# Kernel optimization log

Hardware: AMD Instinct MI355X
Metric: run time of the kernel (lower is better)

The kernel has to match this reference:

```python
import jax, jax.numpy as jnp
import numpy as np

H = 1024
N_IDX = 400000
NBINS = 256


def setup_inputs() -> dict:
    key = jax.random.key(0)
    ks = jax.random.split(key, 10)
    return {
        "input_data": jax.random.uniform(ks[0], (1, 3, H, H), jnp.float32),
        "target_data": jax.random.uniform(ks[1], (1, 3, H, H), jnp.float32) * 2.0 - 1.0,
        "ref": jax.random.uniform(ks[2], (1, 3, H, H), jnp.float32) * 2.0 - 1.0,
        "mask_src": (jax.random.uniform(ks[3], (1, 1, H, H)) > 0.3).astype(jnp.float32) * 255.0,
        "mask_tar": (jax.random.uniform(ks[4], (1, 1, H, H)) > 0.3).astype(jnp.float32) * 255.0,
        "target_data_eye": jax.random.uniform(ks[5], (1, 3, H, H), jnp.float32),
        "idx0": jax.random.randint(ks[6], (N_IDX,), 0, H),
        "idx1": jax.random.randint(ks[7], (N_IDX,), 0, H),
        "idx2": jax.random.randint(ks[8], (N_IDX,), 0, H),
        "idx3": jax.random.randint(ks[9], (N_IDX,), 0, H),
    }


def _cdf(vals):
    # vals: [3, N] float in [0, 256). torch.histc(bins=256, min=0, max=256) -> bin = floor(v)
    bins = jnp.clip(vals.astype(jnp.int32), 0, NBINS - 1)  # [3, N]
    hist = jnp.zeros((3, NBINS), jnp.float32).at[jnp.arange(3)[:, None], bins].add(1.0)
    cdf = jnp.cumsum(hist, axis=1)
    return cdf / cdf[:, -1:]  # normalized cumulative histogram, [3, 256]


def _trans_table(cdf_dst, cdf_ref):
    # cal_trans(ref=cdf_dst, adj=cdf_ref): table[i] = first j in [1,255]
    # with cdf_ref[j-1] <= cdf_dst[i] <= cdf_ref[j]; else table[i] = i; table[255] = 255
    r = cdf_dst[:, None]                  # [256, 1]
    lo = cdf_ref[None, :-1]               # [1, 255] -> adj[j-1], j = 1..255
    hi = cdf_ref[None, 1:]                # [1, 255] -> adj[j]
    cond = (r >= lo) & (r <= hi)          # [256, 255]
    has = cond.any(axis=1)
    j = jnp.argmax(cond, axis=1) + 1      # first matching j
    table = jnp.where(has, j, jnp.arange(NBINS))
    return table.at[NBINS - 1].set(NBINS - 1)


def _hist_match(dst_img, ref_img, i0, i1, i2, i3):
    # dst_img, ref_img: [3, H, W]; gather masked pixels per channel
    dst_align = dst_img[:, i0, i1]        # [3, N]
    ref_align = ref_img[:, i2, i3]        # [3, N]
    cdf_dst = _cdf(dst_align)
    cdf_ref = _cdf(ref_align)
    tables = jax.vmap(_trans_table)(cdf_dst, cdf_ref)  # [3, 256] int
    bins = jnp.clip(dst_align.astype(jnp.int32), 0, NBINS - 1)  # int() truncation, v >= 0
    matched = jnp.take_along_axis(tables, bins, axis=1).astype(dst_img.dtype)  # [3, N]
    return dst_img.at[:, i0, i1].set(matched)


def reference(input_data, target_data, ref, mask_src, mask_tar, target_data_eye,
              idx0, idx1, idx2, idx3):
    # part = 'lip' (generic part) -> histogram_matching branch; use_vgg = False
    de_norm = lambda x: jnp.clip((x + 1.0) / 2.0, 0.0, 1.0)
    target = (de_norm(target_data) * 255.0)[0]          # [3, H, W]
    inp = (jnp.clip(input_data, 0.0, 1.0) * 255.0)[0]   # [3, H, W]
    r = (de_norm(ref) * 255.0)[0]                       # [3, H, W]
    msrc = jnp.broadcast_to(mask_src / 255.0, (1, 3, H, H))[0]
    mtar = jnp.broadcast_to(mask_tar / 255.0, (1, 3, H, H))[0]

    input_masked = inp * msrc
    target_masked = target * mtar
    ref_masked = r * msrc

    input_match = jax.lax.stop_gradient(
        _hist_match(ref_masked, target_masked, idx0, idx1, idx2, idx3))

    loss = jnp.mean(jnp.abs(input_masked / 255.0 - input_match / 255.0))
    return ((target_masked / 255.0)[None], (ref_masked / 255.0)[None],
            (input_masked / 255.0)[None], (input_match / 255.0)[None], loss)
```

## Files before the change

### kernel.cpp

```cpp
#include <hip/hip_runtime.h>

#define H 1024
#define HH (H * H)
#define CHW (3 * HH)
#define NB 256
#define HIST_BLOCKS 768

__device__ __forceinline__ float clamp01(float x) { return fminf(fmaxf(x, 0.0f), 1.0f); }

__device__ __forceinline__ unsigned int bin8(float v01) {
    int b = (int)(v01 * 255.0f);
    return (unsigned int)min(max(b, 0), NB - 1);
}

__global__ void k_elementwise(const float4* __restrict__ inp,
                              const float4* __restrict__ tar,
                              const float4* __restrict__ rfp,
                              const float4* __restrict__ msrc,
                              const float4* __restrict__ mtar,
                              float4* __restrict__ out0, float4* __restrict__ out1,
                              float4* __restrict__ out2, float4* __restrict__ out3,
                              uint4* __restrict__ pk_dst, uint4* __restrict__ pk_ref,
                              unsigned int* __restrict__ gz, float* __restrict__ loss)
{
    if (blockIdx.x == 0) {
        for (int i = threadIdx.x; i < 1536; i += blockDim.x) gz[i] = 0u;
        if (threadIdx.x == 0) *loss = 0.0f;
    }
    int p = blockIdx.x * blockDim.x + threadIdx.x;
    if (p >= HH / 4) return;
    float4 ms4 = msrc[p], mt4 = mtar[p];
    float msx = ms4.x / 255.0f, msy = ms4.y / 255.0f, msz = ms4.z / 255.0f, msw = ms4.w / 255.0f;
    float mtx = mt4.x / 255.0f, mty = mt4.y / 255.0f, mtz = mt4.z / 255.0f, mtw = mt4.w / 255.0f;
    unsigned int bd0 = 0, bd1 = 0, bd2 = 0, bd3 = 0;
    unsigned int br0 = 0, br1 = 0, br2 = 0, br3 = 0;
#pragma unroll
    for (int c = 0; c < 3; ++c) {
        int q = c * (HH / 4) + p;
        float4 t = tar[q], r = rfp[q], iv = inp[q];
        float4 o0, o1, o2;
        o0.x = clamp01((t.x + 1.0f) * 0.5f) * mtx;
        o0.y = clamp01((t.y + 1.0f) * 0.5f) * mty;
        o0.z = clamp01((t.z + 1.0f) * 0.5f) * mtz;
        o0.w = clamp01((t.w + 1.0f) * 0.5f) * mtw;
        o1.x = clamp01((r.x + 1.0f) * 0.5f) * msx;
        o1.y = clamp01((r.y + 1.0f) * 0.5f) * msy;
        o1.z = clamp01((r.z + 1.0f) * 0.5f) * msz;
        o1.w = clamp01((r.w + 1.0f) * 0.5f) * msw;
        o2.x = clamp01(iv.x) * msx;
        o2.y = clamp01(iv.y) * msy;
        o2.z = clamp01(iv.z) * msz;
        o2.w = clamp01(iv.w) * msw;
        out0[q] = o0;
        out1[q] = o1;
        out3[q] = o1;
        out2[q] = o2;
        int sh = 8 * c;
        bd0 |= bin8(o1.x) << sh;  bd1 |= bin8(o1.y) << sh;
        bd2 |= bin8(o1.z) << sh;  bd3 |= bin8(o1.w) << sh;
        br0 |= bin8(o0.x) << sh;  br1 |= bin8(o0.y) << sh;
        br2 |= bin8(o0.z) << sh;  br3 |= bin8(o0.w) << sh;
    }
    pk_dst[p] = make_uint4(bd0, bd1, bd2, bd3);
    pk_ref[p] = make_uint4(br0, br1, br2, br3);
}

__global__ void k_hist(const unsigned int* __restrict__ pk_dst,
                       const unsigned int* __restrict__ pk_ref,
                       const int* __restrict__ i0, const int* __restrict__ i1,
                       const int* __restrict__ i2, const int* __restrict__ i3,
                       unsigned int* __restrict__ ghist, int n)
{
    __shared__ unsigned int h[2 * 3 * NB];
    for (int i = threadIdx.x; i < 2 * 3 * NB; i += blockDim.x) h[i] = 0u;
    __syncthreads();

    int lane = threadIdx.x & 63;
    for (int k = blockIdx.x * blockDim.x + threadIdx.x; k < n; k += gridDim.x * blockDim.x) {
        int pd = i0[k] * H + i1[k];
        int pr = i2[k] * H + i3[k];
        unsigned int a = pk_dst[pd];
        unsigned int b = pk_ref[pr];

        unsigned long long mza = __ballot(a == 0u);
        if (a != 0u) {
            atomicAdd(&h[        (a       & 255u)], 1u);
            atomicAdd(&h[  NB + ((a >> 8) & 255u)], 1u);
            atomicAdd(&h[2*NB + ((a >>16) & 255u)], 1u);
        } else if (lane == __ffsll(mza) - 1) {
            unsigned int cnt = (unsigned int)__popcll(mza);
            atomicAdd(&h[0],      cnt);
            atomicAdd(&h[NB],     cnt);
            atomicAdd(&h[2 * NB], cnt);
        }

        unsigned long long mzb = __ballot(b == 0u);
        if (b != 0u) {
            atomicAdd(&h[3*NB + ( b       & 255u)], 1u);
            atomicAdd(&h[4*NB + ((b >> 8) & 255u)], 1u);
            atomicAdd(&h[5*NB + ((b >>16) & 255u)], 1u);
        } else if (lane == __ffsll(mzb) - 1) {
            unsigned int cnt = (unsigned int)__popcll(mzb);
            atomicAdd(&h[3 * NB], cnt);
            atomicAdd(&h[4 * NB], cnt);
            atomicAdd(&h[5 * NB], cnt);
        }
    }
    __syncthreads();
    for (int i = threadIdx.x; i < 2 * 3 * NB; i += blockDim.x) {
        unsigned int v = h[i];
        if (v) atomicAdd(&ghist[i], v);
    }
}

__global__ void k_tables(const uint4* __restrict__ ghist4, float* __restrict__ table)
{
    __shared__ float cdf[6][NB];
    int t = threadIdx.x;
    int wave = t >> 6, lane = t & 63;

    uint4 v = ghist4[wave * 64 + lane];
    unsigned int s0 = v.x;
    unsigned int s1 = s0 + v.y;
    unsigned int s2 = s1 + v.z;
    unsigned int s3 = s2 + v.w;

    unsigned int scan = s3;
#pragma unroll
    for (int off = 1; off < 64; off <<= 1) {
        unsigned int u = (unsigned int)__shfl_up((int)scan, off, 64);
        if (lane >= off) scan += u;
    }
    unsigned int prefix = scan - s3;
    unsigned int total  = (unsigned int)__shfl((int)scan, 63, 64);
    float ft = (float)total;

    cdf[wave][lane * 4 + 0] = (float)(prefix + s0) / ft;
    cdf[wave][lane * 4 + 1] = (float)(prefix + s1) / ft;
    cdf[wave][lane * 4 + 2] = (float)(prefix + s2) / ft;
    cdf[wave][lane * 4 + 3] = (float)(prefix + s3) / ft;
    __syncthreads();

    if (t < NB) {
#pragma unroll
        for (int c = 0; c < 3; ++c) {
            float r = cdf[c][t];
            const float* cr = cdf[3 + c];
            int lo = 1, hi = NB - 1;
#pragma unroll
            for (int it = 0; it < 8; ++it) {
                int mid = (lo + hi) >> 1;
                if (cr[mid] >= r) hi = mid; else lo = mid + 1;
            }
            int jstar = lo - 1;
            int tab = (jstar == 0 && cr[0] > r) ? t : (jstar + 1);
            if (t == NB - 1) tab = NB - 1;
            table[c * NB + t] = (float)tab / 255.0f;
        }
    }
}

__global__ void k_scatter(const unsigned int* __restrict__ pk_dst,
                          const int* __restrict__ i0, const int* __restrict__ i1,
                          const float* __restrict__ table, float* __restrict__ out3, int n)
{
    __shared__ float tl[3 * NB];
    for (int i = threadIdx.x; i < 3 * NB; i += blockDim.x) tl[i] = table[i];
    __syncthreads();
    int k = blockIdx.x * blockDim.x + threadIdx.x;
    if (k >= n) return;
    int pd = i0[k] * H + i1[k];
    unsigned int a = pk_dst[pd];
    out3[         pd] = tl[        (a       & 255u)];
    out3[HH     + pd] = tl[  NB + ((a >> 8) & 255u)];
    out3[2 * HH + pd] = tl[2*NB + ((a >>16) & 255u)];
}

__global__ void k_loss(const float4* __restrict__ a, const float4* __restrict__ b,
                       float* __restrict__ loss)
{
    float s = 0.0f;
    int n4 = CHW / 4;
    for (int i = blockIdx.x * blockDim.x + threadIdx.x; i < n4; i += gridDim.x * blockDim.x) {
        float4 x = a[i], y = b[i];
        s += fabsf(x.x - y.x) + fabsf(x.y - y.y) + fabsf(x.z - y.z) + fabsf(x.w - y.w);
    }
#pragma unroll
    for (int off = 32; off > 0; off >>= 1) s += __shfl_down(s, off);
    __shared__ float ws[4];
    int lane = threadIdx.x & 63, w = threadIdx.x >> 6;
    if (lane == 0) ws[w] = s;
    __syncthreads();
    if (threadIdx.x == 0) {
        float tsum = ws[0] + ws[1] + ws[2] + ws[3];
        atomicAdd(loss, tsum * (1.0f / (float)CHW));
    }
}

extern "C" void kernel_launch(void* const* d_in, const int* in_sizes, int n_in,
                              void* d_out, int out_size, void* d_ws, size_t ws_size,
                              hipStream_t stream)
{
    const float* inp  = (const float*)d_in[0];
    const float* tar  = (const float*)d_in[1];
    const float* rfp  = (const float*)d_in[2];
    const float* msrc = (const float*)d_in[3];
    const float* mtar = (const float*)d_in[4];
    const int* i0 = (const int*)d_in[6];
    const int* i1 = (const int*)d_in[7];
    const int* i2 = (const int*)d_in[8];
    const int* i3 = (const int*)d_in[9];
    int n = in_sizes[6];

    float* out0 = (float*)d_out;
    float* out1 = out0 + CHW;
    float* out2 = out1 + CHW;
    float* out3 = out2 + CHW;
    float* loss = out3 + CHW;

    unsigned int* ghist  = (unsigned int*)d_ws;
    float*        table  = (float*)((char*)d_ws + 8192);
    unsigned int* pk_dst = (unsigned int*)((char*)d_ws + 16384);
    unsigned int* pk_ref = pk_dst + HH;

    k_elementwise<<<(HH / 4 + 255) / 256, 256, 0, stream>>>(
        (const float4*)inp, (const float4*)tar, (const float4*)rfp,
        (const float4*)msrc, (const float4*)mtar,
        (float4*)out0, (float4*)out1, (float4*)out2, (float4*)out3,
        (uint4*)pk_dst, (uint4*)pk_ref, ghist, loss);

    k_hist<<<HIST_BLOCKS, 512, 0, stream>>>(pk_dst, pk_ref, i0, i1, i2, i3, ghist, n);

    k_tables<<<1, 384, 0, stream>>>((const uint4*)ghist, table);

    k_scatter<<<(n + 255) / 256, 256, 0, stream>>>(pk_dst, i0, i1, table, out3, n);

    k_loss<<<768, 256, 0, stream>>>((const float4*)out2, (const float4*)out3, loss);
}
```

Before: 188.6 us.

## Fuse table build, scatter and loss into one finalize pass using a pixel bitmap

The histogram kernel now also records which destination pixels are scattered into, as bits in a 1M-bit bitmap cleared by the elementwise kernel. A single finalize kernel rebuilds the transfer tables in every block, then streams out1 and, for each pixel, writes either the remapped table value or the original, while accumulating the L1 loss. This removes the separate out3 copy write in the elementwise pass, the scatter kernel, the k_tables launch and a re-read of out3 for the loss. In exchange it adds an atomicOr per index in the histogram pass, and each of the 512 blocks redoes the scan and binary search.

```diff
diff --git a/kernel.cpp b/kernel.cpp
--- a/kernel.cpp
+++ b/kernel.cpp
@@ -5,6 +5,7 @@
 #define CHW (3 * HH)
 #define NB 256
 #define HIST_BLOCKS 768
+#define FIN_BLOCKS 512
 
 __device__ __forceinline__ float clamp01(float x) { return fminf(fmaxf(x, 0.0f), 1.0f); }
 
@@ -19,13 +20,18 @@
                               const float4* __restrict__ msrc,
                               const float4* __restrict__ mtar,
                               float4* __restrict__ out0, float4* __restrict__ out1,
-                              float4* __restrict__ out2, float4* __restrict__ out3,
+                              float4* __restrict__ out2,
                               uint4* __restrict__ pk_dst, uint4* __restrict__ pk_ref,
-                              unsigned int* __restrict__ gz, float* __restrict__ loss)
+                              unsigned int* __restrict__ gz,
+                              unsigned int* __restrict__ bm,
+                              float* __restrict__ loss)
 {
     if (blockIdx.x == 0) {
         for (int i = threadIdx.x; i < 1536; i += blockDim.x) gz[i] = 0u;
         if (threadIdx.x == 0) *loss = 0.0f;
+    } else if (blockIdx.x <= 32) {
+        int base = (int)(blockIdx.x - 1) * 1024;
+        for (int i = threadIdx.x; i < 1024; i += blockDim.x) bm[base + i] = 0u;
     }
     int p = blockIdx.x * blockDim.x + threadIdx.x;
     if (p >= HH / 4) return;
@@ -53,7 +59,6 @@
         o2.w = clamp01(iv.w) * msw;
         out0[q] = o0;
         out1[q] = o1;
-        out3[q] = o1;
         out2[q] = o2;
         int sh = 8 * c;
         bd0 |= bin8(o1.x) << sh;  bd1 |= bin8(o1.y) << sh;
@@ -69,7 +74,8 @@
                        const unsigned int* __restrict__ pk_ref,
                        const int* __restrict__ i0, const int* __restrict__ i1,
                        const int* __restrict__ i2, const int* __restrict__ i3,
-                       unsigned int* __restrict__ ghist, int n)
+                       unsigned int* __restrict__ ghist,
+                       unsigned int* __restrict__ bm, int n)
 {
     __shared__ unsigned int h[2 * 3 * NB];
     for (int i = threadIdx.x; i < 2 * 3 * NB; i += blockDim.x) h[i] = 0u;
@@ -81,6 +87,8 @@
         int pr = i2[k] * H + i3[k];
         unsigned int a = pk_dst[pd];
         unsigned int b = pk_ref[pr];
+
+        atomicOr(&bm[(unsigned int)pd >> 5], 1u << (pd & 31));
 
         unsigned long long mza = __ballot(a == 0u);
         if (a != 0u) {
@@ -113,9 +121,17 @@
     }
 }
 
-__global__ void k_tables(const uint4* __restrict__ ghist4, float* __restrict__ table)
+__global__ __launch_bounds__(384)
+void k_finalize(const uint4* __restrict__ ghist4,
+                const unsigned int* __restrict__ bm,
+                const float4* __restrict__ out1v,
+                const float4* __restrict__ out2v,
+                float4* __restrict__ out3v,
+                float* __restrict__ loss)
 {
     __shared__ float cdf[6][NB];
+    __shared__ float tl[3 * NB];
+    __shared__ float ws[6];
     int t = threadIdx.x;
     int wave = t >> 6, lane = t & 63;
 
@@ -155,44 +171,35 @@
             int jstar = lo - 1;
             int tab = (jstar == 0 && cr[0] > r) ? t : (jstar + 1);
             if (t == NB - 1) tab = NB - 1;
-            table[c * NB + t] = (float)tab / 255.0f;
-        }
-    }
-}
-
-__global__ void k_scatter(const unsigned int* __restrict__ pk_dst,
-                          const int* __restrict__ i0, const int* __restrict__ i1,
-                          const float* __restrict__ table, float* __restrict__ out3, int n)
-{
-    __shared__ float tl[3 * NB];
-    for (int i = threadIdx.x; i < 3 * NB; i += blockDim.x) tl[i] = table[i];
-    __syncthreads();
-    int k = blockIdx.x * blockDim.x + threadIdx.x;
-    if (k >= n) return;
-    int pd = i0[k] * H + i1[k];
-    unsigned int a = pk_dst[pd];
-    out3[         pd] = tl[        (a       & 255u)];
-    out3[HH     + pd] = tl[  NB + ((a >> 8) & 255u)];
-    out3[2 * HH + pd] = tl[2*NB + ((a >>16) & 255u)];
-}
-
-__global__ void k_loss(const float4* __restrict__ a, const float4* __restrict__ b,
-                       float* __restrict__ loss)
-{
+            tl[c * NB + t] = (float)tab / 255.0f;
+        }
+    }
+    __syncthreads();
+
     float s = 0.0f;
-    int n4 = CHW / 4;
-    for (int i = blockIdx.x * blockDim.x + threadIdx.x; i < n4; i += gridDim.x * blockDim.x) {
-        float4 x = a[i], y = b[i];
-        s += fabsf(x.x - y.x) + fabsf(x.y - y.y) + fabsf(x.z - y.z) + fabsf(x.w - y.w);
+    const int n4 = HH / 4;
+    for (int k = blockIdx.x * blockDim.x + t; k < n4; k += gridDim.x * blockDim.x) {
+        unsigned int w = bm[k >> 3];
+        unsigned int nib = (w >> ((k & 7) * 4)) & 0xFu;
+#pragma unroll
+        for (int c = 0; c < 3; ++c) {
+            float4 a = out1v[c * n4 + k];
+            float4 b = out2v[c * n4 + k];
+            float4 o;
+            o.x = (nib & 1u) ? tl[c * NB + bin8(a.x)] : a.x;
+            o.y = (nib & 2u) ? tl[c * NB + bin8(a.y)] : a.y;
+            o.z = (nib & 4u) ? tl[c * NB + bin8(a.z)] : a.z;
+            o.w = (nib & 8u) ? tl[c * NB + bin8(a.w)] : a.w;
+            out3v[c * n4 + k] = o;
+            s += fabsf(b.x - o.x) + fabsf(b.y - o.y) + fabsf(b.z - o.z) + fabsf(b.w - o.w);
+        }
     }
 #pragma unroll
     for (int off = 32; off > 0; off >>= 1) s += __shfl_down(s, off);
-    __shared__ float ws[4];
-    int lane = threadIdx.x & 63, w = threadIdx.x >> 6;
-    if (lane == 0) ws[w] = s;
-    __syncthreads();
-    if (threadIdx.x == 0) {
-        float tsum = ws[0] + ws[1] + ws[2] + ws[3];
+    if (lane == 0) ws[wave] = s;
+    __syncthreads();
+    if (t == 0) {
+        float tsum = ws[0] + ws[1] + ws[2] + ws[3] + ws[4] + ws[5];
         atomicAdd(loss, tsum * (1.0f / (float)CHW));
     }
 }
@@ -219,21 +226,19 @@
     float* loss = out3 + CHW;
 
     unsigned int* ghist  = (unsigned int*)d_ws;
-    float*        table  = (float*)((char*)d_ws + 8192);
-    unsigned int* pk_dst = (unsigned int*)((char*)d_ws + 16384);
+    unsigned int* bm     = (unsigned int*)((char*)d_ws + 8192);
+    unsigned int* pk_dst = (unsigned int*)((char*)d_ws + 139264);
     unsigned int* pk_ref = pk_dst + HH;
 
     k_elementwise<<<(HH / 4 + 255) / 256, 256, 0, stream>>>(
         (const float4*)inp, (const float4*)tar, (const float4*)rfp,
         (const float4*)msrc, (const float4*)mtar,
-        (float4*)out0, (float4*)out1, (float4*)out2, (float4*)out3,
-        (uint4*)pk_dst, (uint4*)pk_ref, ghist, loss);
-
-    k_hist<<<HIST_BLOCKS, 512, 0, stream>>>(pk_dst, pk_ref, i0, i1, i2, i3, ghist, n);
-
-    k_tables<<<1, 384, 0, stream>>>((const uint4*)ghist, table);
-
-    k_scatter<<<(n + 255) / 256, 256, 0, stream>>>(pk_dst, i0, i1, table, out3, n);
-
-    k_loss<<<768, 256, 0, stream>>>((const float4*)out2, (const float4*)out3, loss);
-}
+        (float4*)out0, (float4*)out1, (float4*)out2,
+        (uint4*)pk_dst, (uint4*)pk_ref, ghist, bm, loss);
+
+    k_hist<<<HIST_BLOCKS, 512, 0, stream>>>(pk_dst, pk_ref, i0, i1, i2, i3, ghist, bm, n);
+
+    k_finalize<<<FIN_BLOCKS, 384, 0, stream>>>(
+        (const uint4*)ghist, bm, (const float4*)out1, (const float4*)out2,
+        (float4*)out3, loss);
+}
```

Measured after the change: 175.2 us. -7.1%, faster.
